# Optimization experiments

Hardware: AMD Instinct MI355X
Metric: run time of the kernel (lower is better)

Reference implementation:

```python
import jax, jax.numpy as jnp
import numpy as np

N = 8192
IN_F = 128
OUT_F = 64
ALPHA = 0.2  # LeakyReLU negative slope
NEG_BIG = -9e15

def _xavier(key, shape, gain=1.414):
    fan_in, fan_out = shape[0], shape[1]
    limit = gain * np.sqrt(6.0 / (fan_in + fan_out))
    return jax.random.uniform(key, shape, jnp.float32, -limit, limit)

def setup_inputs() -> dict:
    key = jax.random.key(0)
    k1, k2, k3, k4 = jax.random.split(key, 4)
    h = jax.random.normal(k1, (N, IN_F), jnp.float32)
    adj = jax.random.randint(k2, (N, N), 0, 2, jnp.int32)
    W = _xavier(k3, (IN_F, OUT_F))
    a = _xavier(k4, (2 * OUT_F, 1))
    return {"h": h, "adj": adj, "W": W, "a": a}

def reference(h, adj, W, a):
    Wh = h @ W                                  # [N, OUT_F]
    a1 = a[:OUT_F, 0]                           # [OUT_F]
    a2 = a[OUT_F:, 0]                           # [OUT_F]
    e = (Wh @ a1)[:, None] + (Wh @ a2)[None, :] # [N, N] additive score
    e = jnp.where(e > 0, e, ALPHA * e)          # LeakyReLU
    e = jnp.where(adj > 0, e, NEG_BIG)          # mask non-edges
    attention = jax.nn.softmax(e, axis=1)       # [N, N]
    h_prime = attention @ Wh                    # [N, OUT_F]
    return jax.nn.elu(h_prime)                  # concat=True path
```

## Files before the change

kernel.cpp:

```cpp
#include <hip/hip_runtime.h>
#include <hip/hip_bf16.h>
#include <math.h>

#define NN 8192
#define INF_ 128
#define OUTF 64

typedef __attribute__((ext_vector_type(4))) float f32x4;
typedef __attribute__((ext_vector_type(2))) int i32x2;
typedef __attribute__((ext_vector_type(4))) int i32x4;
typedef __attribute__((ext_vector_type(8))) unsigned short u16x8;
typedef __attribute__((ext_vector_type(8))) __bf16 bf16x8;

#define BAR()                                                    \
    {                                                            \
        asm volatile("s_waitcnt lgkmcnt(0)" ::: "memory");       \
        __builtin_amdgcn_s_barrier();                            \
    }

__device__ __forceinline__ unsigned short f2bf(float f) {
    unsigned int u = __float_as_uint(f);
    u = (u + 0x7FFFu + ((u >> 16) & 1u)) >> 16;
    return (unsigned short)u;
}

__global__ __launch_bounds__(256) void prep_kernel(
    const float* __restrict__ h, const float* __restrict__ W,
    const float* __restrict__ a, unsigned short* __restrict__ WhT,
    float* __restrict__ f1, float* __restrict__ f2)
{
    __shared__ float W_lds[INF_ * OUTF];
    __shared__ float h_lds[32 * INF_];
    __shared__ unsigned short t_lds[OUTF * 34];

    const int t = threadIdx.x;
    const int rb = blockIdx.x * 32;

    {
        const float4* Ws = (const float4*)W;
        float4* Wd = (float4*)W_lds;
        #pragma unroll
        for (int q = 0; q < 8; ++q) Wd[t + 256 * q] = Ws[t + 256 * q];
        const float4* hs = (const float4*)(h + (size_t)rb * INF_);
        float4* hd = (float4*)h_lds;
        #pragma unroll
        for (int q = 0; q < 4; ++q) hd[t + 256 * q] = hs[t + 256 * q];
    }
    __syncthreads();

    const int lane = t & 63;
    const int w = t >> 6;

    float acc[8];
    #pragma unroll
    for (int q = 0; q < 8; ++q) acc[q] = 0.f;
    for (int k = 0; k < INF_; ++k) {
        const float wv = W_lds[k * OUTF + lane];
        #pragma unroll
        for (int q = 0; q < 8; ++q)
            acc[q] = fmaf(h_lds[(w * 8 + q) * INF_ + k], wv, acc[q]);
    }

    const float a1 = a[lane];
    const float a2 = a[OUTF + lane];
    #pragma unroll
    for (int q = 0; q < 8; ++q) {
        float s1 = acc[q] * a1;
        float s2 = acc[q] * a2;
        #pragma unroll
        for (int m = 1; m < 64; m <<= 1) {
            s1 += __shfl_xor(s1, m, 64);
            s2 += __shfl_xor(s2, m, 64);
        }
        if (lane == 0) {
            f1[rb + w * 8 + q] = s1;
            f2[rb + w * 8 + q] = s2;
        }
        t_lds[lane * 34 + w * 8 + q] = f2bf(acc[q]);
    }
    __syncthreads();
    {
        const int c = t >> 2;
        const int ro = (t & 3) * 8;
        unsigned int pk[4];
        #pragma unroll
        for (int i = 0; i < 4; ++i) {
            const unsigned int lo = t_lds[c * 34 + ro + 2 * i];
            const unsigned int hi = t_lds[c * 34 + ro + 2 * i + 1];
            pk[i] = lo | (hi << 16);
        }
        *(uint4*)(WhT + (size_t)c * NN + rb + ro) = make_uint4(pk[0], pk[1], pk[2], pk[3]);
    }
}

__global__ __launch_bounds__(1024) void fmax_kernel(
    const float* __restrict__ f2, float* __restrict__ f2max)
{
    __shared__ float red[16];
    const int t = threadIdx.x;
    float m = -INFINITY;
    #pragma unroll
    for (int q = 0; q < NN / 1024; ++q) m = fmaxf(m, f2[t + q * 1024]);
    #pragma unroll
    for (int s = 1; s < 64; s <<= 1) m = fmaxf(m, __shfl_xor(m, s, 64));
    if ((t & 63) == 0) red[t >> 6] = m;
    __syncthreads();
    if (t == 0) {
        float r = red[0];
        #pragma unroll
        for (int i = 1; i < 16; ++i) r = fmaxf(r, red[i]);
        f2max[0] = r;
    }
}

__global__ __launch_bounds__(256) void repack_kernel(
    const unsigned short* __restrict__ WhT, unsigned short* __restrict__ WhTs)
{
    const int ch = blockIdx.x;
    const int t = threadIdx.x;
    const int qd = t >> 6, l = t & 63;
    const int r = l & 15, g = l >> 4;
    const u16x8 v = *(const u16x8*)(WhT + (size_t)(qd * 16 + r) * NN + ch * 32 + g * 8);
    *(u16x8*)(WhTs + (size_t)ch * 2048 + qd * 512 + l * 8) = v;
}

__global__ __launch_bounds__(512) void gatz_kernel(
    const int* __restrict__ adj, const unsigned short* __restrict__ WhTs,
    const float* __restrict__ f1, const float* __restrict__ f2,
    const float* __restrict__ f2max, float* __restrict__ out)
{
    __shared__ float acc_lds[8 * 16 * OUTF];
    __shared__ float f2_lds[NN];
    __shared__ float l_lds[8 * 16];

    const int t = threadIdx.x;
    const int lane = t & 63;
    const int w = t >> 6;
    const int r = lane & 15;
    const int g = lane >> 4;
    const int row_base = blockIdx.x * 16;

    #pragma unroll
    for (int q = 0; q < 4; ++q)
        ((float4*)f2_lds)[t + 512 * q] = ((const float4*)f2)[t + 512 * q];

    const float f1r = f1[row_base + r];
    float Mr = f1r + f2max[0];
    Mr = fmaxf(Mr, 0.2f * Mr);
    const float nM = -Mr * 1.44269504f;

    f32x4 accl = {0.f, 0.f, 0.f, 0.f};
    f32x4 acc[4];
    #pragma unroll
    for (int q = 0; q < 4; ++q) acc[q] = accl;

    u16x8 ones_u;
    #pragma unroll
    for (int i = 0; i < 8; ++i) ones_u[i] = 0x3F80;
    const bf16x8 bones = __builtin_bit_cast(bf16x8, ones_u);

    const int j0 = w * 1024;
    const int* base = adj + (size_t)row_base * NN + j0 + 2 * lane;
    const u16x8* wv = (const u16x8*)WhTs + lane;

    i32x2 st[16];
    #pragma unroll
    for (int rr = 0; rr < 16; ++rr)
        st[rr] = *(const i32x2*)(base + (size_t)rr * NN);

    BAR();

    for (int s = 0; s < 8; ++s) {
        unsigned long long k0 = 0ull, k1 = 0ull;
        #pragma unroll
        for (int rr = 0; rr < 16; ++rr) {
            const i32x2 v = st[rr];
            const unsigned long long b0 = __ballot(v[0] > 0);
            const unsigned long long b1 = __ballot(v[1] > 0);
            if (rr == r) { k0 = b0; k1 = b1; }
        }
        if (s + 1 < 8) {
            #pragma unroll
            for (int rr = 0; rr < 16; ++rr)
                st[rr] = *(const i32x2*)(base + (size_t)rr * NN + (s + 1) * 128);
        }
        #pragma unroll
        for (int cc = 0; cc < 4; ++cc) {
            const int jl = s * 128 + cc * 32;
            const int col = j0 + jl + g * 8;
            const int ch = (j0 + jl) >> 5;
            const unsigned int sh = 16 * cc + 4 * g;
            const unsigned int m0 = (unsigned int)(k0 >> sh) & 0xFu;
            const unsigned int m1 = (unsigned int)(k1 >> sh) & 0xFu;
            const float4 fa = *(const float4*)(f2_lds + col);
            const float4 fb = *(const float4*)(f2_lds + col + 4);
            const float f2v[8] = {fa.x, fa.y, fa.z, fa.w, fb.x, fb.y, fb.z, fb.w};

            u16x8 pb;
            #pragma unroll
            for (int i = 0; i < 8; ++i) {
                const float e = f1r + f2v[i];
                const float le = fmaxf(e, 0.2f * e);
                float pv = exp2f(fmaf(le, 1.44269504f, nM));
                const unsigned int bit = (((i & 1) ? m1 : m0) >> (i >> 1)) & 1u;
                pv = bit ? pv : 0.f;
                pb[i] = __builtin_bit_cast(unsigned short, __float2bfloat16(pv));
            }

            const bf16x8 af = __builtin_bit_cast(bf16x8, pb);
            #pragma unroll
            for (int qd = 0; qd < 4; ++qd) {
                const bf16x8 bq = __builtin_bit_cast(bf16x8, wv[((size_t)ch * 4 + qd) * 64]);
                acc[qd] = __builtin_amdgcn_mfma_f32_16x16x32_bf16(af, bq, acc[qd], 0, 0, 0);
            }
            accl = __builtin_amdgcn_mfma_f32_16x16x32_bf16(af, bones, accl, 0, 0, 0);
        }
    }

    if (r == 0) {
        #pragma unroll
        for (int q = 0; q < 4; ++q) l_lds[w * 16 + 4 * g + q] = accl[q];
    }
    #pragma unroll
    for (int q = 0; q < 4; ++q) {
        const int m = 4 * g + q;
        #pragma unroll
        for (int qd = 0; qd < 4; ++qd)
            acc_lds[(w * 16 + m) * OUTF + qd * 16 + r] = acc[qd][q];
    }
    __syncthreads();

    {
        #pragma unroll
        for (int hh = 0; hh < 2; ++hh) {
            const int idx = t + hh * 512;
            const int row = idx >> 6;
            const int col = idx & 63;
            float L = 0.f, o = 0.f;
            #pragma unroll
            for (int ww = 0; ww < 8; ++ww) {
                L += l_lds[ww * 16 + row];
                o += acc_lds[(ww * 16 + row) * OUTF + col];
            }
            o /= L;
            o = (o > 0.f) ? o : expm1f(o);
            out[(size_t)(row_base + row) * OUTF + col] = o;
        }
    }
}

extern "C" void kernel_launch(void* const* d_in, const int* in_sizes, int n_in,
                              void* d_out, int out_size, void* d_ws, size_t ws_size,
                              hipStream_t stream) {
    const float* h = (const float*)d_in[0];
    const int* adj = (const int*)d_in[1];
    const float* W = (const float*)d_in[2];
    const float* a = (const float*)d_in[3];
    float* out = (float*)d_out;

    char* ws = (char*)d_ws;
    unsigned short* WhT = (unsigned short*)ws;
    unsigned short* WhTs = (unsigned short*)(ws + (1 << 20));
    float* f1 = (float*)(ws + (2 << 20));
    float* f2 = f1 + NN;
    float* f2m = f2 + NN;

    prep_kernel<<<NN / 32, 256, 0, stream>>>(h, W, a, WhT, f1, f2);
    fmax_kernel<<<1, 1024, 0, stream>>>(f2, f2m);
    repack_kernel<<<NN / 32, 256, 0, stream>>>(WhT, WhTs);
    gatz_kernel<<<NN / 16, 512, 0, stream>>>(adj, WhTs, f1, f2, f2m, out);
}
```

Baseline: 78.85 us.

## Factor attention exponent into precomputed per-column exp values to avoid per-element exp

The per-element exp(leakyrelu(f1+f2)-M) is split into a per-row factor times a per-column factor. A new kernel precomputes exp(f2) and exp(0.2*f2) as packed bf16 pairs, and the main kernel now does a compare-select and one multiply instead of an exp2. The branch of LeakyReLU is picked by comparing the bf16 exp(f2) against a per-row threshold exp(-f1). This removes transcendental work from the inner loop. In exchange it adds a small launch, bf16 rounding in the precomputed factors, and possible overflow or underflow for large f2 or f1 values.

```diff
diff --git a/kernel.cpp b/kernel.cpp
--- a/kernel.cpp
+++ b/kernel.cpp
@@ -8,7 +8,6 @@
 
 typedef __attribute__((ext_vector_type(4))) float f32x4;
 typedef __attribute__((ext_vector_type(2))) int i32x2;
-typedef __attribute__((ext_vector_type(4))) int i32x4;
 typedef __attribute__((ext_vector_type(8))) unsigned short u16x8;
 typedef __attribute__((ext_vector_type(8))) __bf16 bf16x8;
 
@@ -124,13 +123,23 @@
     *(u16x8*)(WhTs + (size_t)ch * 2048 + qd * 512 + l * 8) = v;
 }
 
+__global__ __launch_bounds__(1024) void bd_kernel(
+    const float* __restrict__ f2, unsigned int* __restrict__ bd)
+{
+    const int i = blockIdx.x * 1024 + threadIdx.x;
+    const float v = f2[i];
+    const unsigned int B = f2bf(expf(v));
+    const unsigned int D = f2bf(expf(0.2f * v));
+    bd[i] = B | (D << 16);
+}
+
 __global__ __launch_bounds__(512) void gatz_kernel(
     const int* __restrict__ adj, const unsigned short* __restrict__ WhTs,
-    const float* __restrict__ f1, const float* __restrict__ f2,
+    const float* __restrict__ f1, const unsigned int* __restrict__ bd,
     const float* __restrict__ f2max, float* __restrict__ out)
 {
     __shared__ float acc_lds[8 * 16 * OUTF];
-    __shared__ float f2_lds[NN];
+    __shared__ unsigned int bd_lds[NN];
     __shared__ float l_lds[8 * 16];
 
     const int t = threadIdx.x;
@@ -142,12 +151,14 @@
 
     #pragma unroll
     for (int q = 0; q < 4; ++q)
-        ((float4*)f2_lds)[t + 512 * q] = ((const float4*)f2)[t + 512 * q];
+        ((uint4*)bd_lds)[t + 512 * q] = ((const uint4*)bd)[t + 512 * q];
 
     const float f1r = f1[row_base + r];
     float Mr = f1r + f2max[0];
     Mr = fmaxf(Mr, 0.2f * Mr);
-    const float nM = -Mr * 1.44269504f;
+    const float A = expf(f1r - Mr);
+    const float C = expf(0.2f * f1r - Mr);
+    const unsigned int THb = (unsigned int)f2bf(expf(-f1r));
 
     f32x4 accl = {0.f, 0.f, 0.f, 0.f};
     f32x4 acc[4];
@@ -192,19 +203,23 @@
             const unsigned int sh = 16 * cc + 4 * g;
             const unsigned int m0 = (unsigned int)(k0 >> sh) & 0xFu;
             const unsigned int m1 = (unsigned int)(k1 >> sh) & 0xFu;
-            const float4 fa = *(const float4*)(f2_lds + col);
-            const float4 fb = *(const float4*)(f2_lds + col + 4);
-            const float f2v[8] = {fa.x, fa.y, fa.z, fa.w, fb.x, fb.y, fb.z, fb.w};
+            const uint4 bq0 = *(const uint4*)(bd_lds + col);
+            const uint4 bq1 = *(const uint4*)(bd_lds + col + 4);
+            const unsigned int bdv[8] = {bq0.x, bq0.y, bq0.z, bq0.w,
+                                         bq1.x, bq1.y, bq1.z, bq1.w};
 
             u16x8 pb;
             #pragma unroll
             for (int i = 0; i < 8; ++i) {
-                const float e = f1r + f2v[i];
-                const float le = fmaxf(e, 0.2f * e);
-                float pv = exp2f(fmaf(le, 1.44269504f, nM));
+                const unsigned int v = bdv[i];
+                const unsigned int bb = v & 0xFFFFu;
+                const bool up = bb > THb;
+                const unsigned int sel = up ? bb : (v >> 16);
+                const float f = __uint_as_float(sel << 16);
+                const float as = up ? A : C;
                 const unsigned int bit = (((i & 1) ? m1 : m0) >> (i >> 1)) & 1u;
-                pv = bit ? pv : 0.f;
-                pb[i] = __builtin_bit_cast(unsigned short, __float2bfloat16(pv));
+                const float p = bit ? f * as : 0.f;
+                pb[i] = __builtin_bit_cast(unsigned short, __float2bfloat16(p));
             }
 
             const bf16x8 af = __builtin_bit_cast(bf16x8, pb);
@@ -264,9 +279,11 @@
     float* f1 = (float*)(ws + (2 << 20));
     float* f2 = f1 + NN;
     float* f2m = f2 + NN;
+    unsigned int* bd = (unsigned int*)(f2m + 64);
 
     prep_kernel<<<NN / 32, 256, 0, stream>>>(h, W, a, WhT, f1, f2);
     fmax_kernel<<<1, 1024, 0, stream>>>(f2, f2m);
+    bd_kernel<<<NN / 1024, 1024, 0, stream>>>(f2, bd);
     repack_kernel<<<NN / 32, 256, 0, stream>>>(WhT, WhTs);
-    gatz_kernel<<<NN / 16, 512, 0, stream>>>(adj, WhTs, f1, f2, f2m, out);
-}
+    gatz_kernel<<<NN / 16, 512, 0, stream>>>(adj, WhTs, f1, bd, f2m, out);
+}
```

New measurement: 76.77 us, median of 2. 2.6% less time.
